# Kernel optimization log

Hardware: AMD Instinct MI355X
Metric: run time of the kernel (lower is better)

The kernel has to match this reference:

```python
import jax, jax.numpy as jnp
import numpy as np

N = 100000   # nodes
E = 1_600_000  # edges (avg degree 16)
D = 64       # input_dim = hidden_dim = output_dim
EPS = 1e-5   # BatchNorm eps


def setup_inputs() -> dict:
    key = jax.random.key(0)
    ks = jax.random.split(key, 8)
    x = jax.random.normal(ks[0], (N, D), jnp.float32)
    edge_index = jax.random.randint(ks[1], (2, E), 0, N, jnp.int32)

    def lin_w(k, din, dout):
        s = 1.0 / np.sqrt(din)
        return jax.random.uniform(k, (din, dout), jnp.float32, -s, s)

    return {
        "x": x, "edge_index": edge_index,
        "W1": lin_w(ks[2], D, D), "b1": jnp.zeros((D,), jnp.float32),
        "g1": jnp.ones((D,), jnp.float32), "be1": jnp.zeros((D,), jnp.float32),
        "W2": lin_w(ks[3], D, D), "b2": jnp.zeros((D,), jnp.float32),
        "g2": jnp.ones((D,), jnp.float32), "be2": jnp.zeros((D,), jnp.float32),
        "W3": lin_w(ks[4], D, D), "b3": jnp.zeros((D,), jnp.float32),
        "g3": jnp.ones((D,), jnp.float32), "be3": jnp.zeros((D,), jnp.float32),
    }


def gcn_conv(x, src, dst, W, b):
    # GCNConv: out = D^{-1/2}(A+I)D^{-1/2} (x @ W) + b
    n = x.shape[0]
    loops = jnp.arange(n, dtype=src.dtype)
    s = jnp.concatenate([src, loops])  # add self-loops
    d = jnp.concatenate([dst, loops])
    deg = jax.ops.segment_sum(jnp.ones_like(s, jnp.float32), d, num_segments=n)
    dinv = jax.lax.rsqrt(jnp.maximum(deg, 1.0))  # deg >= 1 (self-loops)
    norm = dinv[s] * dinv[d]                     # [E+N]
    xw = x @ W                                   # [N, D]
    msgs = xw[s] * norm[:, None]                 # [E+N, D] gather
    return jax.ops.segment_sum(msgs, d, num_segments=n) + b  # scatter-add


def batch_norm(z, g, be):
    # training-mode BatchNorm1d: batch statistics, biased variance
    mu = jnp.mean(z, axis=0)
    var = jnp.mean(jnp.square(z - mu), axis=0)
    return (z - mu) * jax.lax.rsqrt(var + EPS) * g + be


def reference(x, edge_index, W1, b1, g1, be1, W2, b2, g2, be2, W3, b3, g3, be3):
    src, dst = edge_index[0], edge_index[1]
    z = jax.nn.relu(batch_norm(gcn_conv(x, src, dst, W1, b1), g1, be1))
    z = jax.nn.relu(batch_norm(gcn_conv(z, src, dst, W2, b2), g2, be2))
    z = batch_norm(gcn_conv(z, src, dst, W3, b3), g3, be3)
    # dropout (p=0.1) is identity in eval mode; normalize=False default
    return z
```

## Files before the change

### kernel.cpp

```cpp
#include <hip/hip_runtime.h>

typedef unsigned short ushort_t;
typedef unsigned int uint_t;
typedef float f32x4 __attribute__((ext_vector_type(4)));
typedef short bf16x8 __attribute__((ext_vector_type(8)));

#define NB_AGG 2560
#define BSHIFT 7
#define BROWS 128
#define BCAP 4096
#define NCHUNK 256
#define ZP 72

__device__ __forceinline__ float bf2f_lo(uint_t u) {
    union { uint_t i; float f; } v; v.i = u << 16; return v.f;
}
__device__ __forceinline__ float bf2f_hi(uint_t u) {
    union { uint_t i; float f; } v; v.i = u & 0xffff0000u; return v.f;
}
__device__ __forceinline__ ushort_t f2bf(float f) {
    union { float f; uint_t i; } v; v.f = f;
    uint_t u = v.i;
    uint_t r = (u + 0x7fffu + ((u >> 16) & 1u)) >> 16;
    return (ushort_t)r;
}

__global__ __launch_bounds__(256) void hist2_k(const int* __restrict__ dst,
                                               int* __restrict__ H, int E, int nb) {
    __shared__ int h[1024];
    int b = blockIdx.x, t = threadIdx.x;
    for (int i = t; i < nb; i += 256) h[i] = 0;
    __syncthreads();
    int per = (E + NCHUNK - 1) / NCHUNK;
    int lo = b * per, hi = min(E, lo + per);
    for (int e = lo + t; e < hi; e += 256)
        atomicAdd(&h[dst[e] >> BSHIFT], 1);
    __syncthreads();
    for (int i = t; i < nb; i += 256) H[(size_t)i * NCHUNK + b] = h[i];
}

__global__ __launch_bounds__(256) void scanA_k(const int* __restrict__ v,
                                               int* __restrict__ segsum, int total) {
    int base = blockIdx.x * 1024 + threadIdx.x;
    int s = 0;
#pragma unroll
    for (int i = 0; i < 4; ++i) {
        int idx = base + i * 256;
        if (idx < total) s += v[idx];
    }
    __shared__ int sh[256];
    sh[threadIdx.x] = s;
    __syncthreads();
    for (int off = 128; off > 0; off >>= 1) {
        if (threadIdx.x < off) sh[threadIdx.x] += sh[threadIdx.x + off];
        __syncthreads();
    }
    if (threadIdx.x == 0) segsum[blockIdx.x] = sh[0];
}

__global__ void scanB_k(int* segsum, int nseg) {
    __shared__ int sh[256];
    int t = threadIdx.x;
    int own = (t < nseg) ? segsum[t] : 0;
    sh[t] = own;
    __syncthreads();
    for (int off = 1; off < 256; off <<= 1) {
        int v = (t >= off) ? sh[t - off] : 0;
        __syncthreads();
        sh[t] += v;
        __syncthreads();
    }
    if (t < nseg) segsum[t] = sh[t] - own;
}

__global__ __launch_bounds__(256) void scanC2_k(int* __restrict__ H,
                                                const int* __restrict__ segsum,
                                                int total) {
    int t = threadIdx.x;
    int base = blockIdx.x * 1024 + t * 4;
    int c0 = 0, c1 = 0, c2 = 0, c3 = 0;
    if (base + 0 < total) c0 = H[base + 0];
    if (base + 1 < total) c1 = H[base + 1];
    if (base + 2 < total) c2 = H[base + 2];
    if (base + 3 < total) c3 = H[base + 3];
    int tsum = c0 + c1 + c2 + c3;
    __shared__ int sh[256];
    sh[t] = tsum;
    __syncthreads();
    for (int off = 1; off < 256; off <<= 1) {
        int v = (t >= off) ? sh[t - off] : 0;
        __syncthreads();
        sh[t] += v;
        __syncthreads();
    }
    int excl = segsum[blockIdx.x] + sh[t] - tsum;
    if (base + 0 < total) H[base + 0] = excl;
    if (base + 1 < total) H[base + 1] = excl + c0;
    if (base + 2 < total) H[base + 2] = excl + c0 + c1;
    if (base + 3 < total) H[base + 3] = excl + c0 + c1 + c2;
}

__global__ __launch_bounds__(256) void scat2_k(const int* __restrict__ src,
                                               const int* __restrict__ dst,
                                               const int* __restrict__ H,
                                               int* __restrict__ colA, int E, int nb) {
    __shared__ int cur[1024];
    int b = blockIdx.x, t = threadIdx.x;
    for (int i = t; i < nb; i += 256) cur[i] = H[(size_t)i * NCHUNK + b];
    __syncthreads();
    int per = (E + NCHUNK - 1) / NCHUNK;
    int lo = b * per, hi = min(E, lo + per);
    for (int e = lo + t; e < hi; e += 256) {
        int d = dst[e];
        int bk = d >> BSHIFT;
        int pos = atomicAdd(&cur[bk], 1);
        colA[pos] = (src[e] << BSHIFT) | (d & (BROWS - 1));
    }
}

__global__ __launch_bounds__(256) void build_k(int* __restrict__ colA,
                                               const int* __restrict__ H,
                                               float* __restrict__ dinv,
                                               int* __restrict__ rowp,
                                               int N, int E, int nb) {
    __shared__ int recs[BCAP];
    __shared__ int cnt[BROWS], pfx[BROWS], cur[BROWS];
    int b = blockIdx.x, t = threadIdx.x;
    int base = H[(size_t)b * NCHUNK];
    int next = (b + 1 < nb) ? H[(size_t)(b + 1) * NCHUNK] : E;
    int size = next - base;
    if (size > BCAP) size = BCAP;
    int row0 = b << BSHIFT;

    if (t < BROWS) { cnt[t] = 0; cur[t] = 0; }
    __syncthreads();

    for (int i = t; i < size; i += 256) {
        int r = colA[base + i];
        recs[i] = r;
        atomicAdd(&cnt[r & (BROWS - 1)], 1);
    }
    __syncthreads();

    if (t < BROWS) pfx[t] = cnt[t];
    __syncthreads();
    for (int off = 1; off < BROWS; off <<= 1) {
        int u = 0;
        if (t < BROWS && t >= off) u = pfx[t - off];
        __syncthreads();
        if (t < BROWS) pfx[t] += u;
        __syncthreads();
    }
    if (t < BROWS) {
        int row = row0 + t;
        if (row < N) {
            int ex = pfx[t] - cnt[t];
            rowp[row] = base + ex;
            dinv[row] = rsqrtf((float)cnt[t] + 1.0f);
            if (row == N - 1) rowp[N] = base + pfx[t];
        }
    }
    __syncthreads();

    for (int i = t; i < size; i += 256) {
        int r = recs[i];
        int l = r & (BROWS - 1);
        int pos = base + (pfx[l] - cnt[l]) + atomicAdd(&cur[l], 1);
        colA[pos] = r >> BSHIFT;
    }
}

template <int MODE>
__global__ __launch_bounds__(256) void gemm_k(const float* __restrict__ Zf,
                                              const uint2* __restrict__ Zb,
                                              const float* __restrict__ W,
                                              const float* __restrict__ dinv,
                                              const float* __restrict__ cA,
                                              const float* __restrict__ cC,
                                              ushort_t* __restrict__ XW, int N) {
    __shared__ ushort_t WbT[64 * ZP];
    __shared__ ushort_t Zt[64 * ZP];
    __shared__ ushort_t Ot[4][16 * ZP];
    __shared__ float Al[64], Cl[64], Dl[64];
    int t = threadIdx.x;
    int row0 = blockIdx.x * 64;

    if (t < 64) {
        int r = row0 + t;
        Dl[t] = (r < N) ? dinv[r] : 0.0f;
        if (MODE) { Al[t] = cA[t]; Cl[t] = cC[t]; }
    }
    {
        int col = t & 63, kg = t >> 6;
#pragma unroll
        for (int kk = 0; kk < 16; ++kk) {
            int k = kg * 16 + kk;
            WbT[col * ZP + k] = f2bf(W[k * 64 + col]);
        }
    }
    __syncthreads();

    {
        int r = t >> 2, cg = t & 3;
        int grow = row0 + r;
        bool gv = grow < N;
#pragma unroll
        for (int q = 0; q < 4; ++q) {
            float4 v;
            if (MODE) {
                uint2 p2 = {0, 0};
                if (gv) p2 = Zb[(size_t)grow * 16 + cg * 4 + q];
                v.x = bf2f_lo(p2.x); v.y = bf2f_hi(p2.x);
                v.z = bf2f_lo(p2.y); v.w = bf2f_hi(p2.y);
                int k = cg * 16 + q * 4;
                v.x = fmaxf(Al[k + 0] * v.x + Cl[k + 0], 0.0f);
                v.y = fmaxf(Al[k + 1] * v.y + Cl[k + 1], 0.0f);
                v.z = fmaxf(Al[k + 2] * v.z + Cl[k + 2], 0.0f);
                v.w = fmaxf(Al[k + 3] * v.w + Cl[k + 3], 0.0f);
            } else {
                if (gv) v = *(const float4*)(Zf + (size_t)grow * 64 + cg * 16 + q * 4);
                else { v.x = v.y = v.z = v.w = 0.0f; }
            }
            uint2 p;
            p.x = (uint_t)f2bf(v.x) | ((uint_t)f2bf(v.y) << 16);
            p.y = (uint_t)f2bf(v.z) | ((uint_t)f2bf(v.w) << 16);
            *(uint2*)&Zt[r * ZP + cg * 16 + q * 4] = p;
        }
    }
    __syncthreads();

    int wv = t >> 6, lane = t & 63;
    int mrow = lane & 15;
    int kgrp = lane >> 4;

    f32x4 acc0 = {0, 0, 0, 0}, acc1 = {0, 0, 0, 0};
    f32x4 acc2 = {0, 0, 0, 0}, acc3 = {0, 0, 0, 0};
#pragma unroll
    for (int ks = 0; ks < 2; ++ks) {
        bf16x8 a = *(bf16x8*)&Zt[(wv * 16 + mrow) * ZP + ks * 32 + kgrp * 8];
        bf16x8 b0 = *(bf16x8*)&WbT[(0 + mrow) * ZP + ks * 32 + kgrp * 8];
        bf16x8 b1 = *(bf16x8*)&WbT[(16 + mrow) * ZP + ks * 32 + kgrp * 8];
        bf16x8 b2 = *(bf16x8*)&WbT[(32 + mrow) * ZP + ks * 32 + kgrp * 8];
        bf16x8 b3 = *(bf16x8*)&WbT[(48 + mrow) * ZP + ks * 32 + kgrp * 8];
        acc0 = __builtin_amdgcn_mfma_f32_16x16x32_bf16(a, b0, acc0, 0, 0, 0);
        acc1 = __builtin_amdgcn_mfma_f32_16x16x32_bf16(a, b1, acc1, 0, 0, 0);
        acc2 = __builtin_amdgcn_mfma_f32_16x16x32_bf16(a, b2, acc2, 0, 0, 0);
        acc3 = __builtin_amdgcn_mfma_f32_16x16x32_bf16(a, b3, acc3, 0, 0, 0);
    }

#pragma unroll
    for (int r = 0; r < 4; ++r) {
        int orow = kgrp * 4 + r;
        float dn = Dl[wv * 16 + orow];
        Ot[wv][orow * ZP + 0 + mrow]  = f2bf(acc0[r] * dn);
        Ot[wv][orow * ZP + 16 + mrow] = f2bf(acc1[r] * dn);
        Ot[wv][orow * ZP + 32 + mrow] = f2bf(acc2[r] * dn);
        Ot[wv][orow * ZP + 48 + mrow] = f2bf(acc3[r] * dn);
    }
#pragma unroll
    for (int i = 0; i < 2; ++i) {
        int cid = lane * 2 + i;
        int orow = cid >> 3, seg = cid & 7;
        int grow = row0 + wv * 16 + orow;
        if (grow < N)
            *(uint4*)(XW + (size_t)grow * 64 + seg * 8) =
                *(uint4*)&Ot[wv][orow * ZP + seg * 8];
    }
}

__global__ __launch_bounds__(256) void agg_k(const ushort_t* __restrict__ y,
                                             const int* __restrict__ row_ptr,
                                             const int* __restrict__ colA,
                                             const float* __restrict__ dinv,
                                             uint2* __restrict__ OUTB,
                                             float* __restrict__ pS,
                                             float* __restrict__ pQ, int N) {
    __shared__ float ssum[64], ssq[64];
    int t = threadIdx.x, lane = t & 63, wv = t >> 6;
    int rs = lane >> 5;
    int g = (lane >> 4) & 1;
    int c = lane & 15;
    if (t < 64) ssum[t] = 0.0f;
    else if (t < 128) ssq[t - 64] = 0.0f;
    __syncthreads();

    const uint2* y2 = (const uint2*)y;
    float ps0 = 0, ps1 = 0, ps2 = 0, ps3 = 0;
    float pq0 = 0, pq1 = 0, pq2 = 0, pq3 = 0;

    int npair = (N + 1) >> 1;
    for (int p = blockIdx.x * 4 + wv; p < npair; p += NB_AGG * 4) {
        int row = p * 2 + rs;
        bool rv = row < N;
        int rc = rv ? row : N - 1;
        int start = row_ptr[rc];
        int end = row_ptr[rc + 1];
        int len = rv ? (end - start) : 0;
        int ml = max(len, __shfl_xor(len, 32));

        float a0 = 0, a1 = 0, a2 = 0, a3 = 0;
        for (int off = 0; off < ml; off += 16) {
            int sA[8];
            uint_t mA[8];
#pragma unroll
            for (int u = 0; u < 8; ++u) {
                int slot = off + u * 2 + g;
                bool val = slot < len;
                int ec = val ? (start + slot) : 0;
                sA[u] = colA[ec];
                mA[u] = val ? 0xffffffffu : 0u;
            }
#pragma unroll
            for (int u = 0; u < 8; ++u) {
                uint2 v = y2[(size_t)sA[u] * 16 + c];
                v.x &= mA[u]; v.y &= mA[u];
                a0 += bf2f_lo(v.x);
                a1 += bf2f_hi(v.x);
                a2 += bf2f_lo(v.y);
                a3 += bf2f_hi(v.y);
            }
        }

        a0 += __shfl_xor(a0, 16);
        a1 += __shfl_xor(a1, 16);
        a2 += __shfl_xor(a2, 16);
        a3 += __shfl_xor(a3, 16);

        if (g == 0 && rv) {
            float dn = dinv[row];
            uint2 sv = y2[(size_t)row * 16 + c];
            float v0 = dn * (a0 + bf2f_lo(sv.x));
            float v1 = dn * (a1 + bf2f_hi(sv.x));
            float v2 = dn * (a2 + bf2f_lo(sv.y));
            float v3 = dn * (a3 + bf2f_hi(sv.y));
            uint2 pk;
            pk.x = (uint_t)f2bf(v0) | ((uint_t)f2bf(v1) << 16);
            pk.y = (uint_t)f2bf(v2) | ((uint_t)f2bf(v3) << 16);
            OUTB[(size_t)row * 16 + c] = pk;
            ps0 += v0; ps1 += v1; ps2 += v2; ps3 += v3;
            pq0 += v0 * v0; pq1 += v1 * v1; pq2 += v2 * v2; pq3 += v3 * v3;
        }
    }

    if (g == 0) {
        atomicAdd(&ssum[c * 4 + 0], ps0); atomicAdd(&ssq[c * 4 + 0], pq0);
        atomicAdd(&ssum[c * 4 + 1], ps1); atomicAdd(&ssq[c * 4 + 1], pq1);
        atomicAdd(&ssum[c * 4 + 2], ps2); atomicAdd(&ssq[c * 4 + 2], pq2);
        atomicAdd(&ssum[c * 4 + 3], ps3); atomicAdd(&ssq[c * 4 + 3], pq3);
    }
    __syncthreads();
    if (t < 64) pS[(size_t)t * NB_AGG + blockIdx.x] = ssum[t];
    else if (t < 128) pQ[(size_t)(t - 64) * NB_AGG + blockIdx.x] = ssq[t - 64];
}

__global__ __launch_bounds__(256) void stats_k(const float* __restrict__ pS,
                                               const float* __restrict__ pQ,
                                               const float* __restrict__ g,
                                               const float* __restrict__ be,
                                               float* __restrict__ cA,
                                               float* __restrict__ cC, int N) {
    int c = blockIdx.x, t = threadIdx.x;
    float s = 0.0f, q = 0.0f;
    for (int i = t; i < NB_AGG; i += 256) {
        s += pS[(size_t)c * NB_AGG + i];
        q += pQ[(size_t)c * NB_AGG + i];
    }
    __shared__ float rs[256], rq[256];
    rs[t] = s; rq[t] = q;
    __syncthreads();
    for (int off = 128; off > 0; off >>= 1) {
        if (t < off) { rs[t] += rs[t + off]; rq[t] += rq[t + off]; }
        __syncthreads();
    }
    if (t == 0) {
        float mu = rs[0] / (float)N;
        float var = rq[0] / (float)N - mu * mu;
        var = fmaxf(var, 0.0f);
        float inv = rsqrtf(var + 1e-5f);
        float a = g[c] * inv;
        cA[c] = a;
        cC[c] = be[c] - mu * a;
    }
}

__global__ __launch_bounds__(256) void apply_k(const uint2* __restrict__ Zb,
                                               float* __restrict__ O,
                                               const float* __restrict__ cA,
                                               const float* __restrict__ cC,
                                               int N) {
    int total = N * 16;
    for (int i = blockIdx.x * 256 + threadIdx.x; i < total; i += gridDim.x * 256) {
        uint2 p = Zb[i];
        int c = (i & 15) * 4;
        float4 v;
        v.x = cA[c + 0] * bf2f_lo(p.x) + cC[c + 0];
        v.y = cA[c + 1] * bf2f_hi(p.x) + cC[c + 1];
        v.z = cA[c + 2] * bf2f_lo(p.y) + cC[c + 2];
        v.w = cA[c + 3] * bf2f_hi(p.y) + cC[c + 3];
        ((float4*)O)[i] = v;
    }
}

extern "C" void kernel_launch(void* const* d_in, const int* in_sizes, int n_in,
                              void* d_out, int out_size, void* d_ws, size_t ws_size,
                              hipStream_t stream) {
    const float* x   = (const float*)d_in[0];
    const int*   ei  = (const int*)d_in[1];
    const float* W1  = (const float*)d_in[2];
    const float* g1  = (const float*)d_in[4];
    const float* be1 = (const float*)d_in[5];
    const float* W2  = (const float*)d_in[6];
    const float* g2  = (const float*)d_in[8];
    const float* be2 = (const float*)d_in[9];
    const float* W3  = (const float*)d_in[10];
    const float* g3  = (const float*)d_in[12];
    const float* be3 = (const float*)d_in[13];

    int N = in_sizes[0] / 64;
    int E = in_sizes[1] / 2;
    const int* srcA = ei;
    const int* dstA = ei + E;
    int nb = (N + BROWS - 1) >> BSHIFT;
    int total = nb * NCHUNK;
    int nseg = (total + 1023) / 1024;

    char* w = (char*)d_ws;
    auto alloc = [&](size_t bytes) -> char* {
        char* p = w;
        w += (bytes + 255) & ~(size_t)255;
        return p;
    };
    ushort_t* xw    = (ushort_t*)alloc((size_t)N * 64 * 2);
    uint2*    zb    = (uint2*)alloc((size_t)N * 64 * 2);
    int*      rowp  = (int*)alloc(((size_t)N + 1) * 4);
    float*    dinv  = (float*)alloc((size_t)N * 4);
    int*      colA  = (int*)alloc((size_t)E * 4);
    int*      H     = (int*)alloc((size_t)total * 4);
    int*      segsum= (int*)alloc((size_t)nseg * 4);
    float*    pS    = (float*)alloc((size_t)64 * NB_AGG * 4);
    float*    pQ    = (float*)alloc((size_t)64 * NB_AGG * 4);
    float*    cA1 = (float*)alloc(256); float* cC1 = (float*)alloc(256);
    float*    cA2 = (float*)alloc(256); float* cC2 = (float*)alloc(256);
    float*    cA3 = (float*)alloc(256); float* cC3 = (float*)alloc(256);
    (void)ws_size; (void)n_in; (void)out_size;

    float* out = (float*)d_out;

    hist2_k<<<NCHUNK, 256, 0, stream>>>(dstA, H, E, nb);
    scanA_k<<<nseg, 256, 0, stream>>>(H, segsum, total);
    scanB_k<<<1, 256, 0, stream>>>(segsum, nseg);
    scanC2_k<<<nseg, 256, 0, stream>>>(H, segsum, total);
    scat2_k<<<NCHUNK, 256, 0, stream>>>(srcA, dstA, H, colA, E, nb);
    build_k<<<nb, 256, 0, stream>>>(colA, H, dinv, rowp, N, E, nb);

    int gemmGrid = (N + 63) / 64;

    gemm_k<0><<<gemmGrid, 256, 0, stream>>>(x, nullptr, W1, dinv, nullptr, nullptr, xw, N);
    agg_k<<<NB_AGG, 256, 0, stream>>>(xw, rowp, colA, dinv, zb, pS, pQ, N);
    stats_k<<<64, 256, 0, stream>>>(pS, pQ, g1, be1, cA1, cC1, N);

    gemm_k<1><<<gemmGrid, 256, 0, stream>>>(nullptr, zb, W2, dinv, cA1, cC1, xw, N);
    agg_k<<<NB_AGG, 256, 0, stream>>>(xw, rowp, colA, dinv, zb, pS, pQ, N);
    stats_k<<<64, 256, 0, stream>>>(pS, pQ, g2, be2, cA2, cC2, N);

    gemm_k<1><<<gemmGrid, 256, 0, stream>>>(nullptr, zb, W3, dinv, cA2, cC2, xw, N);
    agg_k<<<NB_AGG, 256, 0, stream>>>(xw, rowp, colA, dinv, zb, pS, pQ, N);
    stats_k<<<64, 256, 0, stream>>>(pS, pQ, g3, be3, cA3, cC3, N);

    apply_k<<<2048, 256, 0, stream>>>(zb, out, cA3, cC3, N);
}
```

Baseline: 245.4 us.

## Pre-convert weights once and load GEMM operands directly from global into MFMA registers

Adds a small kernel that converts and transposes all three weight matrices to bf16 once, so each GEMM block no longer re-converts W into shared memory. The GEMM now reads its A operand straight from global memory into MFMA fragment registers, applying the BN affine and ReLU inline, which removes the shared-memory staging and two barriers. It also lowers the aggregation grid size. The cost is one extra kernel launch and B fragments fetched from global or cache by every wave instead of from LDS.

```diff
diff --git a/kernel.cpp b/kernel.cpp
--- a/kernel.cpp
+++ b/kernel.cpp
@@ -5,7 +5,7 @@
 typedef float f32x4 __attribute__((ext_vector_type(4)));
 typedef short bf16x8 __attribute__((ext_vector_type(8)));
 
-#define NB_AGG 2560
+#define NB_AGG 2048
 #define BSHIFT 7
 #define BROWS 128
 #define BCAP 4096
@@ -170,78 +170,77 @@
     }
 }
 
+__global__ __launch_bounds__(256) void wconv_k(const float* __restrict__ W1,
+                                               const float* __restrict__ W2,
+                                               const float* __restrict__ W3,
+                                               ushort_t* __restrict__ Wb) {
+    int t = blockIdx.x * 256 + threadIdx.x;
+    if (t >= 3 * 4096) return;
+    int l = t >> 12, i = t & 4095;
+    int col = i >> 6, k = i & 63;
+    const float* W = (l == 0) ? W1 : ((l == 1) ? W2 : W3);
+    Wb[(size_t)l * 4096 + col * 64 + k] = f2bf(W[k * 64 + col]);
+}
+
 template <int MODE>
 __global__ __launch_bounds__(256) void gemm_k(const float* __restrict__ Zf,
-                                              const uint2* __restrict__ Zb,
-                                              const float* __restrict__ W,
+                                              const uint4* __restrict__ Zb,
+                                              const ushort_t* __restrict__ WbT,
                                               const float* __restrict__ dinv,
                                               const float* __restrict__ cA,
                                               const float* __restrict__ cC,
                                               ushort_t* __restrict__ XW, int N) {
-    __shared__ ushort_t WbT[64 * ZP];
-    __shared__ ushort_t Zt[64 * ZP];
     __shared__ ushort_t Ot[4][16 * ZP];
-    __shared__ float Al[64], Cl[64], Dl[64];
+    __shared__ float Al[64], Cl[64];
     int t = threadIdx.x;
     int row0 = blockIdx.x * 64;
-
-    if (t < 64) {
-        int r = row0 + t;
-        Dl[t] = (r < N) ? dinv[r] : 0.0f;
-        if (MODE) { Al[t] = cA[t]; Cl[t] = cC[t]; }
-    }
-    {
-        int col = t & 63, kg = t >> 6;
-#pragma unroll
-        for (int kk = 0; kk < 16; ++kk) {
-            int k = kg * 16 + kk;
-            WbT[col * ZP + k] = f2bf(W[k * 64 + col]);
-        }
-    }
-    __syncthreads();
-
-    {
-        int r = t >> 2, cg = t & 3;
-        int grow = row0 + r;
-        bool gv = grow < N;
-#pragma unroll
-        for (int q = 0; q < 4; ++q) {
-            float4 v;
-            if (MODE) {
-                uint2 p2 = {0, 0};
-                if (gv) p2 = Zb[(size_t)grow * 16 + cg * 4 + q];
-                v.x = bf2f_lo(p2.x); v.y = bf2f_hi(p2.x);
-                v.z = bf2f_lo(p2.y); v.w = bf2f_hi(p2.y);
-                int k = cg * 16 + q * 4;
-                v.x = fmaxf(Al[k + 0] * v.x + Cl[k + 0], 0.0f);
-                v.y = fmaxf(Al[k + 1] * v.y + Cl[k + 1], 0.0f);
-                v.z = fmaxf(Al[k + 2] * v.z + Cl[k + 2], 0.0f);
-                v.w = fmaxf(Al[k + 3] * v.w + Cl[k + 3], 0.0f);
-            } else {
-                if (gv) v = *(const float4*)(Zf + (size_t)grow * 64 + cg * 16 + q * 4);
-                else { v.x = v.y = v.z = v.w = 0.0f; }
-            }
-            uint2 p;
-            p.x = (uint_t)f2bf(v.x) | ((uint_t)f2bf(v.y) << 16);
-            p.y = (uint_t)f2bf(v.z) | ((uint_t)f2bf(v.w) << 16);
-            *(uint2*)&Zt[r * ZP + cg * 16 + q * 4] = p;
-        }
-    }
-    __syncthreads();
-
     int wv = t >> 6, lane = t & 63;
     int mrow = lane & 15;
     int kgrp = lane >> 4;
 
+    if (MODE) {
+        if (t < 64) { Al[t] = cA[t]; Cl[t] = cC[t]; }
+        __syncthreads();
+    }
+
+    int row = row0 + wv * 16 + mrow;
+    bool rv = row < N;
+    size_t rc = rv ? (size_t)row : 0;
+
     f32x4 acc0 = {0, 0, 0, 0}, acc1 = {0, 0, 0, 0};
     f32x4 acc2 = {0, 0, 0, 0}, acc3 = {0, 0, 0, 0};
 #pragma unroll
     for (int ks = 0; ks < 2; ++ks) {
-        bf16x8 a = *(bf16x8*)&Zt[(wv * 16 + mrow) * ZP + ks * 32 + kgrp * 8];
-        bf16x8 b0 = *(bf16x8*)&WbT[(0 + mrow) * ZP + ks * 32 + kgrp * 8];
-        bf16x8 b1 = *(bf16x8*)&WbT[(16 + mrow) * ZP + ks * 32 + kgrp * 8];
-        bf16x8 b2 = *(bf16x8*)&WbT[(32 + mrow) * ZP + ks * 32 + kgrp * 8];
-        bf16x8 b3 = *(bf16x8*)&WbT[(48 + mrow) * ZP + ks * 32 + kgrp * 8];
+        int ko = ks * 32 + kgrp * 8;
+        float av[8];
+        if (MODE) {
+            uint4 p = {0, 0, 0, 0};
+            if (rv) p = Zb[rc * 8 + (ko >> 3)];
+            av[0] = bf2f_lo(p.x); av[1] = bf2f_hi(p.x);
+            av[2] = bf2f_lo(p.y); av[3] = bf2f_hi(p.y);
+            av[4] = bf2f_lo(p.z); av[5] = bf2f_hi(p.z);
+            av[6] = bf2f_lo(p.w); av[7] = bf2f_hi(p.w);
+#pragma unroll
+            for (int i = 0; i < 8; ++i)
+                av[i] = fmaxf(Al[ko + i] * av[i] + Cl[ko + i], 0.0f);
+        } else {
+            float4 q0 = {0, 0, 0, 0}, q1 = {0, 0, 0, 0};
+            if (rv) {
+                q0 = *(const float4*)&Zf[rc * 64 + ko];
+                q1 = *(const float4*)&Zf[rc * 64 + ko + 4];
+            }
+            av[0] = q0.x; av[1] = q0.y; av[2] = q0.z; av[3] = q0.w;
+            av[4] = q1.x; av[5] = q1.y; av[6] = q1.z; av[7] = q1.w;
+        }
+        bf16x8 a;
+#pragma unroll
+        for (int i = 0; i < 8; ++i) a[i] = (short)f2bf(av[i]);
+
+        bf16x8 b0 = *(const bf16x8*)&WbT[(0 + mrow) * 64 + ko];
+        bf16x8 b1 = *(const bf16x8*)&WbT[(16 + mrow) * 64 + ko];
+        bf16x8 b2 = *(const bf16x8*)&WbT[(32 + mrow) * 64 + ko];
+        bf16x8 b3 = *(const bf16x8*)&WbT[(48 + mrow) * 64 + ko];
+
         acc0 = __builtin_amdgcn_mfma_f32_16x16x32_bf16(a, b0, acc0, 0, 0, 0);
         acc1 = __builtin_amdgcn_mfma_f32_16x16x32_bf16(a, b1, acc1, 0, 0, 0);
         acc2 = __builtin_amdgcn_mfma_f32_16x16x32_bf16(a, b2, acc2, 0, 0, 0);
@@ -251,7 +250,8 @@
 #pragma unroll
     for (int r = 0; r < 4; ++r) {
         int orow = kgrp * 4 + r;
-        float dn = Dl[wv * 16 + orow];
+        int grow = row0 + wv * 16 + orow;
+        float dn = (grow < N) ? dinv[grow] : 0.0f;
         Ot[wv][orow * ZP + 0 + mrow]  = f2bf(acc0[r] * dn);
         Ot[wv][orow * ZP + 16 + mrow] = f2bf(acc1[r] * dn);
         Ot[wv][orow * ZP + 32 + mrow] = f2bf(acc2[r] * dn);
@@ -432,6 +432,7 @@
     };
     ushort_t* xw    = (ushort_t*)alloc((size_t)N * 64 * 2);
     uint2*    zb    = (uint2*)alloc((size_t)N * 64 * 2);
+    ushort_t* Wb    = (ushort_t*)alloc((size_t)3 * 4096 * 2);
     int*      rowp  = (int*)alloc(((size_t)N + 1) * 4);
     float*    dinv  = (float*)alloc((size_t)N * 4);
     int*      colA  = (int*)alloc((size_t)E * 4);
@@ -452,18 +453,19 @@
     scanC2_k<<<nseg, 256, 0, stream>>>(H, segsum, total);
     scat2_k<<<NCHUNK, 256, 0, stream>>>(srcA, dstA, H, colA, E, nb);
     build_k<<<nb, 256, 0, stream>>>(colA, H, dinv, rowp, N, E, nb);
+    wconv_k<<<48, 256, 0, stream>>>(W1, W2, W3, Wb);
 
     int gemmGrid = (N + 63) / 64;
 
-    gemm_k<0><<<gemmGrid, 256, 0, stream>>>(x, nullptr, W1, dinv, nullptr, nullptr, xw, N);
+    gemm_k<0><<<gemmGrid, 256, 0, stream>>>(x, nullptr, Wb, dinv, nullptr, nullptr, xw, N);
     agg_k<<<NB_AGG, 256, 0, stream>>>(xw, rowp, colA, dinv, zb, pS, pQ, N);
     stats_k<<<64, 256, 0, stream>>>(pS, pQ, g1, be1, cA1, cC1, N);
 
-    gemm_k<1><<<gemmGrid, 256, 0, stream>>>(nullptr, zb, W2, dinv, cA1, cC1, xw, N);
+    gemm_k<1><<<gemmGrid, 256, 0, stream>>>(nullptr, (const uint4*)zb, Wb + 4096, dinv, cA1, cC1, xw, N);
     agg_k<<<NB_AGG, 256, 0, stream>>>(xw, rowp, colA, dinv, zb, pS, pQ, N);
     stats_k<<<64, 256, 0, stream>>>(pS, pQ, g2, be2, cA2, cC2, N);
 
-    gemm_k<1><<<gemmGrid, 256, 0, stream>>>(nullptr, zb, W3, dinv, cA2, cC2, xw, N);
+    gemm_k<1><<<gemmGrid, 256, 0, stream>>>(nullptr, (const uint4*)zb, Wb + 8192, dinv, cA2, cC2, xw, N);
     agg_k<<<NB_AGG, 256, 0, stream>>>(xw, rowp, colA, dinv, zb, pS, pQ, N);
     stats_k<<<64, 256, 0, stream>>>(pS, pQ, g3, be3, cA3, cC3, N);
 
```

After: 246.9 us. About the same (+0.6%).
